# Kernel optimization log

Measured on AMD Instinct MI355X. Metric: run time of the kernel, lower is better.

Reference implementation:

```python
import jax, jax.numpy as jnp
import numpy as np

B, T, N, D = 2, 256, 128, 512
H = 8
D_INNER, D_STATE, D_CONV, DT_RANK = 2 * D, 16, 4, D // 16  # mamba defaults
EPS = 1e-5


def setup_inputs() -> dict:
    key = jax.random.key(0)
    ks = iter(jax.random.split(key, 32))
    g = lambda shape, s=0.02: jax.random.normal(next(ks), shape, dtype=jnp.float32) * s
    return {
        "x": jax.random.normal(next(ks), (B, T, N, D), dtype=jnp.float32),
        "mha_in_w": g((3 * D, D)), "mha_in_b": jnp.zeros((3 * D,), jnp.float32),
        "mha_out_w": g((D, D)), "mha_out_b": jnp.zeros((D,), jnp.float32),
        "n1_w": jnp.ones((D,), jnp.float32),
        "n2_w": jnp.ones((D,), jnp.float32),
        "n3_w": jnp.ones((D,), jnp.float32),
        "m_in_w": g((2 * D_INNER, D)),
        "m_conv_w": g((D_INNER, 1, D_CONV), 0.1), "m_conv_b": jnp.zeros((D_INNER,), jnp.float32),
        "m_xproj_w": g((DT_RANK + 2 * D_STATE, D_INNER)),
        "m_dt_w": g((D_INNER, DT_RANK)), "m_dt_b": jnp.full((D_INNER,), -4.6, jnp.float32),
        "m_A_log": jnp.tile(jnp.log(jnp.arange(1, D_STATE + 1, dtype=jnp.float32)), (D_INNER, 1)),
        "m_D": jnp.ones((D_INNER,), jnp.float32),
        "m_out_w": g((D, D_INNER)),
        "mlp_w1": g((2 * D, D)), "mlp_b1": jnp.zeros((2 * D,), jnp.float32),
        "mlp_w2": g((D, 2 * D)), "mlp_b2": jnp.zeros((D,), jnp.float32),
    }


def rmsnorm(x, w):
    return x * jax.lax.rsqrt(jnp.mean(x * x, axis=-1, keepdims=True) + EPS) * w


def mha(x, in_w, in_b, out_w, out_b):
    # x: (Bt, N, D); torch nn.MultiheadAttention with batch_first=True
    Bt, n, d = x.shape
    dh = d // H
    qkv = x @ in_w.T + in_b
    q, k, v = jnp.split(qkv, 3, axis=-1)
    q = q.reshape(Bt, n, H, dh)
    k = k.reshape(Bt, n, H, dh)
    v = v.reshape(Bt, n, H, dh)
    att = jax.nn.softmax(jnp.einsum('bnhd,bmhd->bhnm', q, k) / jnp.sqrt(jnp.float32(dh)), axis=-1)
    o = jnp.einsum('bhnm,bmhd->bnhd', att, v).reshape(Bt, n, d)
    return o @ out_w.T + out_b


def mamba(x, in_w, conv_w, conv_b, xproj_w, dt_w, dt_b, A_log, Dp, out_w):
    # x: (Bm, L, D)  -- standard mamba_ssm Mamba block (expand=2, d_state=16, d_conv=4)
    Bm, L, _ = x.shape
    xz = x @ in_w.T                      # (Bm, L, 2*d_inner)
    xm, z = jnp.split(xz, 2, axis=-1)
    # causal depthwise conv1d along time
    xc = jnp.pad(xm.transpose(0, 2, 1), ((0, 0), (0, 0), (D_CONV - 1, 0)))
    xc = jax.lax.conv_general_dilated(xc, conv_w, (1,), 'VALID',
                                      dimension_numbers=('NCH', 'OIH', 'NCH'),
                                      feature_group_count=D_INNER)
    xm = jax.nn.silu(xc.transpose(0, 2, 1) + conv_b)   # (Bm, L, d_inner)
    x_dbl = xm @ xproj_w.T
    dt, Bs, Cs = jnp.split(x_dbl, [DT_RANK, DT_RANK + D_STATE], axis=-1)
    dt = jax.nn.softplus(dt @ dt_w.T + dt_b)           # (Bm, L, d_inner)
    A = -jnp.exp(A_log)                                # (d_inner, d_state)

    def step(h, inp):
        dt_t, B_t, C_t, u_t = inp                      # (Bm,d_in),(Bm,ds),(Bm,ds),(Bm,d_in)
        dA = jnp.exp(dt_t[:, :, None] * A)             # (Bm, d_inner, d_state)
        h = dA * h + (dt_t * u_t)[:, :, None] * B_t[:, None, :]
        y = jnp.einsum('bds,bs->bd', h, C_t)
        return h, y

    h0 = jnp.zeros((Bm, D_INNER, D_STATE), x.dtype)
    inputs = (dt.transpose(1, 0, 2), Bs.transpose(1, 0, 2),
              Cs.transpose(1, 0, 2), xm.transpose(1, 0, 2))
    _, ys = jax.lax.scan(step, h0, inputs)
    y = ys.transpose(1, 0, 2) + xm * Dp
    y = y * jax.nn.silu(z)
    return y @ out_w.T


def reference(x, mha_in_w, mha_in_b, mha_out_w, mha_out_b, n1_w, n2_w, n3_w,
              m_in_w, m_conv_w, m_conv_b, m_xproj_w, m_dt_w, m_dt_b, m_A_log, m_D, m_out_w,
              mlp_w1, mlp_b1, mlp_w2, mlp_b2):
    Bx, Tx, Nx, Dx = x.shape
    # spatial attention over regions
    xs = x.reshape(Bx * Tx, Nx, Dx)
    xs = rmsnorm(xs + mha(xs, mha_in_w, mha_in_b, mha_out_w, mha_out_b), n1_w)
    # temporal mamba over time
    xt = xs.reshape(Bx, Tx, Nx, Dx).transpose(0, 2, 1, 3).reshape(Bx * Nx, Tx, Dx)
    xt = rmsnorm(xt + mamba(xt, m_in_w, m_conv_w, m_conv_b, m_xproj_w,
                            m_dt_w, m_dt_b, m_A_log, m_D, m_out_w), n2_w)
    # MLP (1 hidden layer, width 2*D, ReLU)
    x3 = xt.reshape(Bx, Nx, Tx, Dx).transpose(0, 2, 1, 3)
    h = jax.nn.relu(x3 @ mlp_w1.T + mlp_b1) @ mlp_w2.T + mlp_b2
    return rmsnorm(x3 + h, n3_w)
```

## Files before the change

### kernel.cpp

```cpp
#include <hip/hip_runtime.h>

typedef unsigned short u16;
typedef unsigned int u32;
typedef __attribute__((ext_vector_type(8))) short short8;
typedef __attribute__((ext_vector_type(4))) float f32x4;

__device__ __forceinline__ float bf2f(u16 u){ union{u32 i; float f;} v; v.i=((u32)u)<<16; return v.f; }
__device__ __forceinline__ u16 f2bf(float f){ union{float f; u32 i;} v; v.f=f; u32 r=v.i+0x7FFFu+((v.i>>16)&1u); return (u16)(r>>16); }

__device__ __forceinline__ void glds16(const u16* g, u16* lds){
  __builtin_amdgcn_global_load_lds((const __attribute__((address_space(1))) u32*)g,
                                   (__attribute__((address_space(3))) u32*)lds, 16, 0, 0);
}

__global__ __launch_bounds__(256) void cvt_kernel(const float* __restrict__ src, u16* __restrict__ dst, int n4){
  int i = blockIdx.x*256 + threadIdx.x;
  if (i >= n4) return;
  float4 v = ((const float4*)src)[i];
  union { u16 o[4]; uint2 q; } t;
  t.o[0]=f2bf(v.x); t.o[1]=f2bf(v.y); t.o[2]=f2bf(v.z); t.o[3]=f2bf(v.w);
  ((uint2*)dst)[i] = t.q;
}

template<int BM, int BN, int EPI>
__global__ __launch_bounds__(256, 3) void gemm_bt_kernel(
    const u16* __restrict__ A, int lda,
    const u16* __restrict__ B,
    const float* __restrict__ bias,
    u16* __restrict__ C, int ldc,
    int N, int K)
{
  constexpr int RM = BM/32, RN = BN/32;
  constexpr int AI = BM/64, BI = BN/64;
  const int tid = threadIdx.x;
  const int wave = tid>>6, lane = tid&63;
  const int wm = wave>>1, wn = wave&1;
  const int lm = lane&15, quad = lane>>4;
  const int bm0 = blockIdx.x*BM, bn0 = blockIdx.y*BN;
  __shared__ __align__(16) u16 As[BM*32];
  __shared__ __align__(16) u16 Bs[BN*32];
  f32x4 acc[RM][RN] = {};
  const int vr = tid>>2, vc = (tid&3)<<3;
  for (int k0=0; k0<K; k0+=32){
    __syncthreads();
    #pragma unroll
    for (int i=0;i<AI;i++)
      glds16(A + (size_t)(bm0 + i*64 + vr)*lda + k0 + vc, &As[(i*256 + wave*64)*8]);
    #pragma unroll
    for (int i=0;i<BI;i++)
      glds16(B + (size_t)(bn0 + i*64 + vr)*K + k0 + vc, &Bs[(i*256 + wave*64)*8]);
    __syncthreads();
    short8 af[RM], bfr[RN];
    #pragma unroll
    for (int i=0;i<RM;i++) af[i] = *(const short8*)(&As[(wm*(BM/2)+i*16+lm)*32 + quad*8]);
    #pragma unroll
    for (int j=0;j<RN;j++) bfr[j] = *(const short8*)(&Bs[(wn*(BN/2)+j*16+lm)*32 + quad*8]);
    #pragma unroll
    for (int i=0;i<RM;i++)
      #pragma unroll
      for (int j=0;j<RN;j++)
        acc[i][j] = __builtin_amdgcn_mfma_f32_16x16x32_bf16(af[i], bfr[j], acc[i][j], 0,0,0);
  }
  #pragma unroll
  for (int j=0;j<RN;j++){
    int col = bn0 + wn*(BN/2) + j*16 + lm;
    float bv = 0.f;
    if (EPI >= 1) bv = bias[col];
    #pragma unroll
    for (int i=0;i<RM;i++){
      int r0 = bm0 + wm*(BM/2) + i*16 + quad*4;
      #pragma unroll
      for (int r=0;r<4;r++){
        float v = acc[i][j][r] + bv;
        if (EPI == 2) v = fmaxf(v, 0.f);
        if (EPI == 3) v = (v > 20.f) ? v : log1pf(__expf(v));
        C[(size_t)(r0+r)*ldc + col] = f2bf(v);
      }
    }
  }
}

__global__ __launch_bounds__(256, 2) void attn_kernel(const u16* __restrict__ qkv, u16* __restrict__ o)
{
  const int bb = blockIdx.x >> 3;
  const int hh = blockIdx.x & 7;
  const int tid = threadIdx.x;
  const int wave = tid>>6, lane = tid&63;
  const int lm = lane&15, quad = lane>>4;
  __shared__ union {
    struct { u16 Q[128][72]; u16 K[128][72]; } qk;
    u16 P[128][136];
  } sm;
  __shared__ __align__(16) u16 Vt[64][136];
  const size_t base = (size_t)bb*128*1536 + (size_t)hh*64;
  #pragma unroll
  for (int i=0;i<4;i++){
    int v = i*256 + tid;
    int r = v>>3, c = (v&7)<<3;
    *(uint4*)(&sm.qk.Q[r][c]) = *(const uint4*)(qkv + base + (size_t)r*1536 + c);
    *(uint4*)(&sm.qk.K[r][c]) = *(const uint4*)(qkv + base + 512 + (size_t)r*1536 + c);
    union { uint4 q; u16 u[8]; } vv;
    vv.q = *(const uint4*)(qkv + base + 1024 + (size_t)r*1536 + c);
    #pragma unroll
    for (int j=0;j<8;j++) Vt[c+j][r] = vv.u[j];
  }
  __syncthreads();
  f32x4 sa[2][8] = {};
  #pragma unroll
  for (int k0=0;k0<64;k0+=32){
    short8 af[2], bfr[8];
    #pragma unroll
    for (int i=0;i<2;i++) af[i] = *(const short8*)(&sm.qk.Q[wave*32+i*16+lm][k0+quad*8]);
    #pragma unroll
    for (int j=0;j<8;j++) bfr[j] = *(const short8*)(&sm.qk.K[j*16+lm][k0+quad*8]);
    #pragma unroll
    for (int i=0;i<2;i++)
      #pragma unroll
      for (int j=0;j<8;j++)
        sa[i][j] = __builtin_amdgcn_mfma_f32_16x16x32_bf16(af[i], bfr[j], sa[i][j], 0,0,0);
  }
  __syncthreads();
  #pragma unroll
  for (int i=0;i<2;i++){
    #pragma unroll
    for (int r=0;r<4;r++){
      float mx = -1e30f;
      #pragma unroll
      for (int j=0;j<8;j++) mx = fmaxf(mx, sa[i][j][r]);
      #pragma unroll
      for (int off=1; off<16; off<<=1) mx = fmaxf(mx, __shfl_xor(mx, off, 64));
      float pv[8]; float sum = 0.f;
      #pragma unroll
      for (int j=0;j<8;j++){ pv[j] = __expf((sa[i][j][r]-mx)*0.125f); sum += pv[j]; }
      #pragma unroll
      for (int off=1; off<16; off<<=1) sum += __shfl_xor(sum, off, 64);
      float inv = 1.f/sum;
      int row = wave*32 + i*16 + quad*4 + r;
      #pragma unroll
      for (int j=0;j<8;j++) sm.P[row][j*16+lm] = f2bf(pv[j]*inv);
    }
  }
  f32x4 oa[2][4] = {};
  #pragma unroll
  for (int k0=0;k0<128;k0+=32){
    short8 af[2], bfr[4];
    #pragma unroll
    for (int i=0;i<2;i++) af[i] = *(const short8*)(&sm.P[wave*32+i*16+lm][k0+quad*8]);
    #pragma unroll
    for (int j=0;j<4;j++) bfr[j] = *(const short8*)(&Vt[j*16+lm][k0+quad*8]);
    #pragma unroll
    for (int i=0;i<2;i++)
      #pragma unroll
      for (int j=0;j<4;j++)
        oa[i][j] = __builtin_amdgcn_mfma_f32_16x16x32_bf16(af[i], bfr[j], oa[i][j], 0,0,0);
  }
  #pragma unroll
  for (int i=0;i<2;i++)
    #pragma unroll
    for (int j=0;j<4;j++){
      int col = hh*64 + j*16 + lm;
      int r0 = wave*32 + i*16 + quad*4;
      #pragma unroll
      for (int r=0;r<4;r++)
        o[(size_t)(bb*128 + r0 + r)*512 + col] = f2bf(oa[i][j][r]);
    }
}

__global__ __launch_bounds__(256) void conv_silu_kernel(const u16* __restrict__ xc,
    const float* __restrict__ cw, const float* __restrict__ cb, u16* __restrict__ xm)
{
  int id = blockIdx.x*256 + threadIdx.x;
  int r = id >> 7, c8 = (id & 127) << 3;
  int t = r & 255;
  union { uint4 q; u16 u[8]; } rv[4];
  #pragma unroll
  for (int tap=0;tap<4;tap++){
    int ts = t - 3 + tap;
    if (ts >= 0) rv[tap].q = *(const uint4*)(xc + (size_t)(r-3+tap)*1024 + c8);
    else rv[tap].q = make_uint4(0,0,0,0);
  }
  union { uint4 q; u16 u[8]; } out;
  #pragma unroll
  for (int j=0;j<8;j++){
    float4 wj = ((const float4*)cw)[c8+j];
    float a = cb[c8+j];
    a += bf2f(rv[0].u[j])*wj.x + bf2f(rv[1].u[j])*wj.y + bf2f(rv[2].u[j])*wj.z + bf2f(rv[3].u[j])*wj.w;
    a = a / (1.f + __expf(-a));
    out.u[j] = f2bf(a);
  }
  *(uint4*)(xm + (size_t)r*1024 + c8) = out.q;
}

typedef union { uint4 q; u16 u[8]; } BC8;
__global__ __launch_bounds__(256) void scan_kernel(
    const u16* dtp, const u16* __restrict__ xm, const u16* __restrict__ xdbl,
    const u16* __restrict__ zp, const float* __restrict__ A_log, const float* __restrict__ Dp,
    u16* yp)
{
  int bm = blockIdx.x;
  int d = blockIdx.y*256 + threadIdx.x;
  float h[16];
  bool fast = true;
  #pragma unroll
  for (int s=0;s<16;s++){
    float a = __expf(A_log[d*16+s]);
    float tgt = (float)(s+1);
    fast = fast && (fabsf(a - tgt) <= 1e-4f*tgt);
    h[s] = 0.f;
  }
  float Dv = Dp[d];
  size_t rowbase = (size_t)bm*256;

  float dtb[2], ub[2], zvb[2];
  BC8 b0b[2], b1b[2], c0b[2], c1b[2];
  #pragma unroll
  for (int j=0;j<2;j++){
    size_t row = rowbase + j;
    dtb[j] = bf2f(dtp[row*1024 + d]);
    ub[j]  = bf2f(xm[row*1024 + d]);
    zvb[j] = bf2f(zp[row*1024 + d]);
    const u16* bc = xdbl + row*64;
    b0b[j].q = *(const uint4*)(bc+32); b1b[j].q = *(const uint4*)(bc+40);
    c0b[j].q = *(const uint4*)(bc+48); c1b[j].q = *(const uint4*)(bc+56);
  }
  #pragma unroll 2
  for (int t=0;t<256;t++){
    const int j = t & 1;
    const float dt = dtb[j], u = ub[j], z = zvb[j];
    const BC8 b0 = b0b[j], b1 = b1b[j], c0 = c0b[j], c1 = c1b[j];
    {
      size_t rown = rowbase + ((t+2) & 255);
      dtb[j] = bf2f(dtp[rown*1024 + d]);
      ub[j]  = bf2f(xm[rown*1024 + d]);
      zvb[j] = bf2f(zp[rown*1024 + d]);
      const u16* bcn = xdbl + rown*64;
      b0b[j].q = *(const uint4*)(bcn+32); b1b[j].q = *(const uint4*)(bcn+40);
      c0b[j].q = *(const uint4*)(bcn+48); c1b[j].q = *(const uint4*)(bcn+56);
    }
    const float du = dt*u;
    float ya[4] = {0.f, 0.f, 0.f, 0.f};
    if (fast){
      float e1 = __expf(-dt);
      float e2=e1*e1, e3=e2*e1, e4=e2*e2, e5=e4*e1, e6=e4*e2, e7=e4*e3, e8=e4*e4;
      float e9=e8*e1, e10=e8*e2, e11=e8*e3, e12=e8*e4, e13=e8*e5, e14=e8*e6, e15=e8*e7, e16=e8*e8;
      float pw[16] = {e1,e2,e3,e4,e5,e6,e7,e8,e9,e10,e11,e12,e13,e14,e15,e16};
      #pragma unroll
      for (int s=0;s<8;s++){
        h[s] = pw[s]*h[s] + du*bf2f(b0.u[s]);
        ya[s&3] += h[s]*bf2f(c0.u[s]);
      }
      #pragma unroll
      for (int s=0;s<8;s++){
        h[8+s] = pw[8+s]*h[8+s] + du*bf2f(b1.u[s]);
        ya[s&3] += h[8+s]*bf2f(c1.u[s]);
      }
    } else {
      #pragma unroll
      for (int s=0;s<8;s++){
        float As = -__expf(A_log[d*16+s]);
        h[s] = __expf(dt*As)*h[s] + du*bf2f(b0.u[s]);
        ya[s&3] += h[s]*bf2f(c0.u[s]);
      }
      #pragma unroll
      for (int s=0;s<8;s++){
        float As = -__expf(A_log[d*16+8+s]);
        h[8+s] = __expf(dt*As)*h[8+s] + du*bf2f(b1.u[s]);
        ya[s&3] += h[8+s]*bf2f(c1.u[s]);
      }
    }
    const float yv = (ya[0]+ya[1]) + (ya[2]+ya[3]);
    const float o = (yv + u*Dv) * (z / (1.f + __expf(-z)));
    yp[(rowbase + t)*1024 + d] = f2bf(o);
  }
}

__global__ __launch_bounds__(256) void transpose_kernel(const u16* __restrict__ in, u16* __restrict__ out){
  int id = blockIdx.x*256 + threadIdx.x;
  int row_out = id >> 6, v = (id & 63) << 3;
  int b = row_out >> 15, rem = row_out & 32767;
  int n = rem >> 8, t = rem & 255;
  int row_in = (b*256 + t)*128 + n;
  *(uint4*)(out + (size_t)row_out*512 + v) = *(const uint4*)(in + (size_t)row_in*512 + v);
}

template<bool RES_F32, bool OUT_F32, bool PERM>
__global__ __launch_bounds__(256) void rmsnorm_kernel(const u16* mn,
    const void* res, const float* __restrict__ w, void* out, int rowoff)
{
  int row = blockIdx.x*4 + (threadIdx.x>>6);
  int lane = threadIdx.x & 63;
  size_t base = (size_t)row*512 + lane*8;
  union { uint4 q; u16 u[8]; } mv;
  mv.q = *(const uint4*)(mn + base);
  float vals[8];
  if (RES_F32){
    const float* rp = (const float*)res + base;
    float4 r0 = ((const float4*)rp)[0];
    float4 r1 = ((const float4*)rp)[1];
    float rr[8] = {r0.x,r0.y,r0.z,r0.w,r1.x,r1.y,r1.z,r1.w};
    #pragma unroll
    for (int j=0;j<8;j++) vals[j] = bf2f(mv.u[j]) + rr[j];
  } else {
    union { uint4 q; u16 u[8]; } rv;
    rv.q = *(const uint4*)((const u16*)res + base);
    #pragma unroll
    for (int j=0;j<8;j++) vals[j] = bf2f(mv.u[j]) + bf2f(rv.u[j]);
  }
  float ss = 0.f;
  #pragma unroll
  for (int j=0;j<8;j++) ss += vals[j]*vals[j];
  #pragma unroll
  for (int off=1; off<64; off<<=1) ss += __shfl_xor(ss, off, 64);
  float sc = rsqrtf(ss*(1.f/512.f) + 1e-5f);
  size_t obase = base;
  if (PERM){
    int g = row + rowoff;
    int p = ((g>>15)<<15) | ((g&255)<<7) | ((g>>8)&127);
    obase = (size_t)p*512 + lane*8;
  }
  if (OUT_F32){
    float* op = (float*)out + obase;
    float o[8];
    #pragma unroll
    for (int j=0;j<8;j++) o[j] = vals[j]*sc*w[lane*8+j];
    ((float4*)op)[0] = make_float4(o[0],o[1],o[2],o[3]);
    ((float4*)op)[1] = make_float4(o[4],o[5],o[6],o[7]);
  } else {
    union { uint4 q; u16 u[8]; } ov;
    #pragma unroll
    for (int j=0;j<8;j++) ov.u[j] = f2bf(vals[j]*sc*w[lane*8+j]);
    *(uint4*)((u16*)out + obase) = ov.q;
  }
}

static size_t req_bytes(int NC){
  size_t R = 65536/NC;
  size_t regB = (R*2048 > 33554432ull) ? R*2048 : 33554432ull;
  return 2ull * (4194304ull + 33554432ull + regB + R*2560ull);
}

extern "C" void kernel_launch(void* const* d_in, const int* in_sizes, int n_in,
                              void* d_out, int out_size, void* d_ws, size_t ws_size,
                              hipStream_t stream)
{
  const float* x       = (const float*)d_in[0];
  const float* w_qkv_f = (const float*)d_in[1];
  const float* b_qkv   = (const float*)d_in[2];
  const float* w_out_f = (const float*)d_in[3];
  const float* b_out   = (const float*)d_in[4];
  const float* n1w     = (const float*)d_in[5];
  const float* n2w     = (const float*)d_in[6];
  const float* n3w     = (const float*)d_in[7];
  const float* w_min_f = (const float*)d_in[8];
  const float* convw   = (const float*)d_in[9];
  const float* convb   = (const float*)d_in[10];
  const float* w_xp_f  = (const float*)d_in[11];
  const float* w_dt_f  = (const float*)d_in[12];
  const float* b_dt    = (const float*)d_in[13];
  const float* A_log   = (const float*)d_in[14];
  const float* Dp      = (const float*)d_in[15];
  const float* w_mo_f  = (const float*)d_in[16];
  const float* w_1_f   = (const float*)d_in[17];
  const float* b_1     = (const float*)d_in[18];
  const float* w_2_f   = (const float*)d_in[19];
  const float* b_2     = (const float*)d_in[20];
  float* out = (float*)d_out;
  u16* wsu = (u16*)d_ws;

  int NC = 16;
  if      (ws_size >= req_bytes(1)) NC = 1;
  else if (ws_size >= req_bytes(2)) NC = 2;
  else if (ws_size >= req_bytes(4)) NC = 4;
  else if (ws_size >= req_bytes(8)) NC = 8;
  const size_t R = 65536/NC;

  u16* w_qkv = wsu;
  u16* w_o   = w_qkv + 786432;
  u16* w_mi  = w_o   + 262144;
  u16* w_xp  = w_mi  + 1048576;
  u16* w_dt  = w_xp  + 65536;
  u16* w_mo  = w_dt  + 32768;
  u16* w_1   = w_mo  + 524288;
  u16* w_2   = w_1   + 524288;
  u16* xt    = wsu + 4194304;
  const size_t baseB = 37748736;
  const size_t regB  = (R*2048 > 33554432ull) ? R*2048 : 33554432ull;
  const size_t baseC = baseB + regB;
  u16* o2    = wsu + baseB;
  u16* zb    = wsu + baseB;
  u16* xmb   = wsu + baseB + R*1024;
  u16* xbf_c = wsu + baseC;
  u16* qkv_c = wsu + baseC + R*512;
  u16* oat_c = wsu + baseC + R*2048;
  u16* slab  = wsu + baseC;
  u16* xdbl_c= wsu + baseC + R*1024;
  u16* mo_c  = wsu + baseC + R*1088;
  u16* h1_c  = wsu + baseC;
  u16* h2_c  = wsu + baseC + R*1024;

  struct CV { const float* s; u16* d; int n; };
  const CV cvs[] = {
    {w_qkv_f, w_qkv, 786432}, {w_out_f, w_o, 262144}, {w_min_f, w_mi, 1048576},
    {w_xp_f, w_xp, 65536}, {w_dt_f, w_dt, 32768}, {w_mo_f, w_mo, 524288},
    {w_1_f, w_1, 524288}, {w_2_f, w_2, 524288},
  };
  for (int i = 0; i < 8; i++){
    int n4 = cvs[i].n / 4;
    cvt_kernel<<<(n4+255)/256, 256, 0, stream>>>(cvs[i].s, cvs[i].d, n4);
  }

  for (int c = 0; c < NC; c++){
    cvt_kernel<<<R/2, 256, 0, stream>>>(x + c*R*512, xbf_c, (int)(R*128));
    gemm_bt_kernel<128,128,1><<<dim3(R/128,12), 256, 0, stream>>>(xbf_c, 512, w_qkv, b_qkv, qkv_c, 1536, 1536, 512);
    attn_kernel<<<(R/128)*8, 256, 0, stream>>>(qkv_c, oat_c);
    gemm_bt_kernel<128,128,1><<<dim3(R/128,4), 256, 0, stream>>>(oat_c, 512, w_o, b_out, o2 + c*R*512, 512, 512, 512);
  }
  rmsnorm_kernel<true,false,false><<<16384, 256, 0, stream>>>(o2, x, n1w, o2, 0);
  transpose_kernel<<<16384, 256, 0, stream>>>(o2, xt);

  for (int c = 0; c < NC; c++){
    const u16* xtc = xt + c*R*512;
    gemm_bt_kernel<128,128,0><<<dim3(R/128,8), 256, 0, stream>>>(xtc, 512, w_mi, nullptr, slab, 1024, 1024, 512);
    gemm_bt_kernel<128,128,0><<<dim3(R/128,8), 256, 0, stream>>>(xtc, 512, w_mi + 524288, nullptr, zb, 1024, 1024, 512);
    conv_silu_kernel<<<R/2, 256, 0, stream>>>(slab, convw, convb, xmb);
    gemm_bt_kernel<64,64,0><<<dim3(R/64,1), 256, 0, stream>>>(xmb, 1024, w_xp, nullptr, xdbl_c, 64, 64, 1024);
    gemm_bt_kernel<128,128,3><<<dim3(R/128,8), 256, 0, stream>>>(xdbl_c, 64, w_dt, b_dt, slab, 1024, 1024, 32);
    scan_kernel<<<dim3(R/256,4), 256, 0, stream>>>(slab, xmb, xdbl_c, zb, A_log, Dp, slab);
    gemm_bt_kernel<128,128,0><<<dim3(R/128,4), 256, 0, stream>>>(slab, 1024, w_mo, nullptr, mo_c, 512, 512, 1024);
    rmsnorm_kernel<false,false,false><<<R/4, 256, 0, stream>>>(mo_c, xtc, n2w, (void*)xtc, 0);
  }

  for (int c = 0; c < NC; c++){
    const u16* x3c = xt + c*R*512;
    gemm_bt_kernel<128,128,2><<<dim3(R/128,8), 256, 0, stream>>>(x3c, 512, w_1, b_1, h1_c, 1024, 1024, 512);
    gemm_bt_kernel<128,128,1><<<dim3(R/128,4), 256, 0, stream>>>(h1_c, 1024, w_2, b_2, h2_c, 512, 512, 1024);
    rmsnorm_kernel<false,true,true><<<R/4, 256, 0, stream>>>(h2_c, x3c, n3w, out, (int)(c*R));
  }
}
```

Measured before the change: 1.864 ms.

## Add 256x256 tile double-buffered GEMM kernel for large projections

Adds a new 512-thread GEMM kernel with 256x256 output tiles, a K-step of 64, double-buffered LDS filled by direct global-to-LDS loads, XOR-swizzled LDS layout, and s_setprio around the MFMA bursts. All large projection GEMMs (QKV, attention out, mamba in/out, MLP) are switched to it. The aim is more data reuse per loaded tile and overlap of loads with MFMA compute. In exchange it uses 128KB of LDS and many accumulator registers, which limits it to one block per CU, and launches fewer blocks, which may hurt occupancy or tail balance.

Result: slower. 1.970 ms (+5.6%).

```diff
diff --git a/kernel.cpp b/kernel.cpp
--- a/kernel.cpp
+++ b/kernel.cpp
@@ -20,6 +20,95 @@
   union { u16 o[4]; uint2 q; } t;
   t.o[0]=f2bf(v.x); t.o[1]=f2bf(v.y); t.o[2]=f2bf(v.z); t.o[3]=f2bf(v.w);
   ((uint2*)dst)[i] = t.q;
+}
+
+template<int EPI>
+__global__ __launch_bounds__(512, 1) void gemm256_kernel(
+    const u16* __restrict__ A, int lda,
+    const u16* __restrict__ B,
+    const float* __restrict__ bias,
+    u16* __restrict__ C, int ldc,
+    int K)
+{
+  const int tid = threadIdx.x;
+  const int wave = tid>>6, lane = tid&63;
+  const int wm = wave>>2, wn = wave&3;
+  const int lm = lane&15, quad = lane>>4;
+  const int bm0 = blockIdx.x*256, bn0 = blockIdx.y*256;
+  __shared__ __align__(16) u16 As[2][16384];
+  __shared__ __align__(16) u16 Bs[2][16384];
+  const int NT = K >> 6;
+  const int srow = wave*8 + (lane>>3);
+  const int scol = ((lane&7) ^ ((lane>>3)&7)) << 3;
+  f32x4 acc[8][4] = {};
+
+  #pragma unroll
+  for (int t=0;t<2;t++){
+    #pragma unroll
+    for (int u=0;u<4;u++){
+      glds16(A + (size_t)(bm0 + u*64 + srow)*lda + t*64 + scol, &As[t][u*4096 + wave*512]);
+      glds16(B + (size_t)(bn0 + u*64 + srow)*K   + t*64 + scol, &Bs[t][u*4096 + wave*512]);
+    }
+  }
+  asm volatile("s_waitcnt vmcnt(8)" ::: "memory");
+  __builtin_amdgcn_s_barrier();
+
+  for (int T=0; T<NT; ++T){
+    const int p = T & 1;
+    short8 bfr[2][4];
+    #pragma unroll
+    for (int ks=0;ks<2;ks++)
+      #pragma unroll
+      for (int j=0;j<4;j++){
+        int row = wn*64 + j*16 + lm;
+        bfr[ks][j] = *(const short8*)(&Bs[p][row*64 + (((ks*4+quad)^(lm&7))<<3)]);
+      }
+    #pragma unroll
+    for (int i=0;i<8;i++){
+      int row = wm*128 + i*16 + lm;
+      short8 a0 = *(const short8*)(&As[p][row*64 + ((quad^(lm&7))<<3)]);
+      short8 a1 = *(const short8*)(&As[p][row*64 + (((4+quad)^(lm&7))<<3)]);
+      __builtin_amdgcn_s_setprio(1);
+      #pragma unroll
+      for (int j=0;j<4;j++){
+        acc[i][j] = __builtin_amdgcn_mfma_f32_16x16x32_bf16(a0, bfr[0][j], acc[i][j], 0,0,0);
+        acc[i][j] = __builtin_amdgcn_mfma_f32_16x16x32_bf16(a1, bfr[1][j], acc[i][j], 0,0,0);
+      }
+      __builtin_amdgcn_s_setprio(0);
+    }
+    if (T+1 < NT){
+      asm volatile("s_waitcnt lgkmcnt(0)" ::: "memory");
+      __builtin_amdgcn_s_barrier();
+      if (T+2 < NT){
+        const int k0 = (T+2)*64;
+        #pragma unroll
+        for (int u=0;u<4;u++){
+          glds16(A + (size_t)(bm0 + u*64 + srow)*lda + k0 + scol, &As[p][u*4096 + wave*512]);
+          glds16(B + (size_t)(bn0 + u*64 + srow)*K   + k0 + scol, &Bs[p][u*4096 + wave*512]);
+        }
+        asm volatile("s_waitcnt vmcnt(8)" ::: "memory");
+      } else {
+        asm volatile("s_waitcnt vmcnt(0)" ::: "memory");
+      }
+      __builtin_amdgcn_s_barrier();
+    }
+  }
+  #pragma unroll
+  for (int j=0;j<4;j++){
+    int col = bn0 + wn*64 + j*16 + lm;
+    float bv = 0.f;
+    if (EPI >= 1) bv = bias[col];
+    #pragma unroll
+    for (int i=0;i<8;i++){
+      int r0 = bm0 + wm*128 + i*16 + quad*4;
+      #pragma unroll
+      for (int r=0;r<4;r++){
+        float v = acc[i][j][r] + bv;
+        if (EPI == 2) v = fmaxf(v, 0.f);
+        C[(size_t)(r0+r)*ldc + col] = f2bf(v);
+      }
+    }
+  }
 }
 
 template<int BM, int BN, int EPI>
@@ -411,29 +500,29 @@
 
   for (int c = 0; c < NC; c++){
     cvt_kernel<<<R/2, 256, 0, stream>>>(x + c*R*512, xbf_c, (int)(R*128));
-    gemm_bt_kernel<128,128,1><<<dim3(R/128,12), 256, 0, stream>>>(xbf_c, 512, w_qkv, b_qkv, qkv_c, 1536, 1536, 512);
+    gemm256_kernel<1><<<dim3(R/256,6), 512, 0, stream>>>(xbf_c, 512, w_qkv, b_qkv, qkv_c, 1536, 512);
     attn_kernel<<<(R/128)*8, 256, 0, stream>>>(qkv_c, oat_c);
-    gemm_bt_kernel<128,128,1><<<dim3(R/128,4), 256, 0, stream>>>(oat_c, 512, w_o, b_out, o2 + c*R*512, 512, 512, 512);
+    gemm256_kernel<1><<<dim3(R/256,2), 512, 0, stream>>>(oat_c, 512, w_o, b_out, o2 + c*R*512, 512, 512);
   }
   rmsnorm_kernel<true,false,false><<<16384, 256, 0, stream>>>(o2, x, n1w, o2, 0);
   transpose_kernel<<<16384, 256, 0, stream>>>(o2, xt);
 
   for (int c = 0; c < NC; c++){
     const u16* xtc = xt + c*R*512;
-    gemm_bt_kernel<128,128,0><<<dim3(R/128,8), 256, 0, stream>>>(xtc, 512, w_mi, nullptr, slab, 1024, 1024, 512);
-    gemm_bt_kernel<128,128,0><<<dim3(R/128,8), 256, 0, stream>>>(xtc, 512, w_mi + 524288, nullptr, zb, 1024, 1024, 512);
+    gemm256_kernel<0><<<dim3(R/256,4), 512, 0, stream>>>(xtc, 512, w_mi, nullptr, slab, 1024, 512);
+    gemm256_kernel<0><<<dim3(R/256,4), 512, 0, stream>>>(xtc, 512, w_mi + 524288, nullptr, zb, 1024, 512);
     conv_silu_kernel<<<R/2, 256, 0, stream>>>(slab, convw, convb, xmb);
     gemm_bt_kernel<64,64,0><<<dim3(R/64,1), 256, 0, stream>>>(xmb, 1024, w_xp, nullptr, xdbl_c, 64, 64, 1024);
     gemm_bt_kernel<128,128,3><<<dim3(R/128,8), 256, 0, stream>>>(xdbl_c, 64, w_dt, b_dt, slab, 1024, 1024, 32);
     scan_kernel<<<dim3(R/256,4), 256, 0, stream>>>(slab, xmb, xdbl_c, zb, A_log, Dp, slab);
-    gemm_bt_kernel<128,128,0><<<dim3(R/128,4), 256, 0, stream>>>(slab, 1024, w_mo, nullptr, mo_c, 512, 512, 1024);
+    gemm256_kernel<0><<<dim3(R/256,2), 512, 0, stream>>>(slab, 1024, w_mo, nullptr, mo_c, 512, 1024);
     rmsnorm_kernel<false,false,false><<<R/4, 256, 0, stream>>>(mo_c, xtc, n2w, (void*)xtc, 0);
   }
 
   for (int c = 0; c < NC; c++){
     const u16* x3c = xt + c*R*512;
-    gemm_bt_kernel<128,128,2><<<dim3(R/128,8), 256, 0, stream>>>(x3c, 512, w_1, b_1, h1_c, 1024, 1024, 512);
-    gemm_bt_kernel<128,128,1><<<dim3(R/128,4), 256, 0, stream>>>(h1_c, 1024, w_2, b_2, h2_c, 512, 512, 1024);
+    gemm256_kernel<2><<<dim3(R/256,4), 512, 0, stream>>>(x3c, 512, w_1, b_1, h1_c, 1024, 512);
+    gemm256_kernel<1><<<dim3(R/256,2), 512, 0, stream>>>(h1_c, 1024, w_2, b_2, h2_c, 512, 1024);
     rmsnorm_kernel<false,true,true><<<R/4, 256, 0, stream>>>(h2_c, x3c, n3w, out, (int)(c*R));
   }
 }
```
